# Kernel optimization log

Measured on AMD Instinct MI355X. Metric: run time of the kernel, lower is better.

Reference implementation:

```python
import jax, jax.numpy as jnp
import numpy as np
import math

ORDER = 4
FREQ = 160


def _layernorm(x, g, b, eps=1e-5):
    m = jnp.mean(x, axis=-1, keepdims=True)
    v = jnp.mean((x - m) ** 2, axis=-1, keepdims=True)
    return (x - m) / jnp.sqrt(v + eps) * g + b


def setup_inputs() -> dict:
    key = jax.random.key(0)
    ks = jax.random.split(key, 9)
    b, t, k, f = 8, 1000, ORDER, FREQ
    return {
        "far_complex": jax.random.normal(ks[0], (b, 2, f, t), jnp.float32),
        "mix_complex": jax.random.normal(ks[1], (b, 2, f, t), jnp.float32),
        "k_conv_w": jax.random.normal(ks[2], (2 * k, 2), jnp.float32) * 0.3,   # Conv2d(2 -> 2k, 1x1)
        "k_conv_b": jax.random.normal(ks[3], (2 * k,), jnp.float32) * 0.01,
        "ql_w": jax.random.normal(ks[4], (f, f), jnp.float32) / math.sqrt(f),  # query_linear
        "ql_b": jnp.zeros((f,), jnp.float32),
        "qn_g": jnp.ones((f,), jnp.float32),   # query_norm gamma
        "qn_b": jnp.zeros((f,), jnp.float32),  # query_norm beta
        "kl_w": jax.random.normal(ks[5], (k, k), jnp.float32) / math.sqrt(k),  # key_linear
        "kl_b": jnp.zeros((k,), jnp.float32),
        "kn_g": jnp.ones((k,), jnp.float32),
        "kn_b": jnp.zeros((k,), jnp.float32),
        "q_vec": jax.random.normal(ks[6], (f,), jnp.float32) * 0.5,  # query_vector
        "k_vec": jax.random.normal(ks[7], (k,), jnp.float32) * 0.5,  # key_vector
        "v_vec": jax.random.normal(ks[8], (k,), jnp.float32) * 0.5,  # value_vector
    }


def reference(far_complex, mix_complex, k_conv_w, k_conv_b, ql_w, ql_b,
              qn_g, qn_b, kl_w, kl_b, kn_g, kn_b, q_vec, k_vec, v_vec):
    b, c, f, t = far_complex.shape
    k = k_vec.shape[0]

    # im2col-style unfold over time with left padding (k-1)
    padded = jnp.pad(far_complex, ((0, 0), (0, 0), (0, 0), (k - 1, 0)))
    idx = jnp.arange(t)[:, None] + jnp.arange(k)[None, :]          # [t, k]
    unf = padded[..., idx]                                          # [b,2,f,t,k]
    unf_save = unf[:, 0] + 1j * unf[:, 1]                           # [b,f,t,k] complex64
    # in-place conjugation of imag channel (as in torch code)
    unf = jnp.stack([unf[:, 0], -unf[:, 1]], axis=1)                # [b,2,f,t,k]

    # per-channel outer products (torch does real matmul per channel)
    XTX = jnp.einsum('bcfti,bcftj->bcftij', unf, unf)               # [b,2,f,t,k,k]
    XTY = (unf * mix_complex[..., None])[..., None]                 # [b,2,f,t,k,1]

    query = jnp.transpose(unf, (0, 1, 3, 4, 2))                     # [b,2,t,k,f]
    kc = jnp.einsum('oc,bcft->boft', k_conv_w, mix_complex) + k_conv_b[None, :, None, None]
    key = jnp.transpose(kc.reshape(b, 2, k, f, t), (0, 1, 4, 3, 2))  # [b,2,t,f,k]

    value = jnp.swapaxes(jnp.concatenate([XTX, XTY], axis=-1), -1, -2)  # [b,2,f,t,k+1,k]

    query = _layernorm(query @ ql_w.T + ql_b, qn_g, qn_b) * jax.nn.sigmoid(q_vec)
    key = _layernorm(key @ kl_w.T + kl_b, kn_g, kn_b) * jax.nn.sigmoid(k_vec)
    value = value * jax.nn.sigmoid(v_vec)

    weight = jax.nn.softmax(query @ (key / math.sqrt(k)), axis=-1)  # [b,2,t,k,k]
    out = value @ weight[:, :, None]                                # [b,2,f,t,k+1,k]
    outT = jnp.swapaxes(out, -1, -2)                                # [b,2,f,t,k,k+1]
    XTX_new = outT[..., :k]                                         # [b,2,f,t,k,k]
    XTY_new = outT[..., k:]                                         # [b,2,f,t,k,1]
    XTX_c = XTX_new[:, 0] + 1j * XTX_new[:, 1]                      # [b,f,t,k,k]
    XTY_c = XTY_new[:, 0] + 1j * XTY_new[:, 1]                      # [b,f,t,k,1]

    eps = 1e-8
    eye_r = jnp.eye(k, dtype=jnp.float32) + eps
    eye = (eye_r + 1j * eye_r).astype(XTX_c.dtype)

    inv_XTX = jnp.linalg.inv(XTX_c + eye)                           # [b,f,t,k,k]
    wiener = (inv_XTX @ XTY_c)[..., 0]                              # [b,f,t,k]

    res = jnp.sum(unf_save * wiener, axis=-1)                       # [b,f,t]
    return jnp.stack([res.real, res.imag], axis=1)                  # [b,2,f,t]
```

## Files before the change

kernel.cpp:

```cpp
#include <hip/hip_runtime.h>
#include <math.h>

#define NBC   16
#define NF    160
#define NT    1000
#define TS    64
#define QSTR  81

typedef __attribute__((ext_vector_type(8))) short short8;
typedef __attribute__((ext_vector_type(4))) float f32x4;

static __device__ __forceinline__ short f2bf(float x) {
    unsigned u = __builtin_bit_cast(unsigned, x);
    unsigned r = (u + 0x7fffu + ((u >> 16) & 1u)) >> 16;
    return (short)r;
}
static __device__ __forceinline__ float bf2f(short s) {
    unsigned u = ((unsigned)(unsigned short)s) << 16;
    return __builtin_bit_cast(float, u);
}

__global__ __launch_bounds__(1024) void k13_fused(const float* __restrict__ far,
                                                  const float* __restrict__ mix,
                                                  const float* __restrict__ qlw,
                                                  const float* __restrict__ qlb,
                                                  const float* __restrict__ qng,
                                                  const float* __restrict__ qnb,
                                                  const float* __restrict__ qvec,
                                                  const float* __restrict__ kcw,
                                                  const float* __restrict__ kcb,
                                                  const float* __restrict__ klw,
                                                  const float* __restrict__ klb,
                                                  const float* __restrict__ kng,
                                                  const float* __restrict__ knb,
                                                  const float* __restrict__ kvec,
                                                  float* __restrict__ W) {
    __shared__ float pool[17600];
    __shared__ float lnM[80], lnI[80];
    float* Qlds = pool;
    float* redS = pool;
    float* redQ = pool + 3280;
    short* Bhi  = (short*)(pool + 12960);
    short* Blo  = (short*)(pool + 14240);
    float* sbuf = pool;

    const int bc = blockIdx.x;
    const int t0 = blockIdx.y * TS;
    const int tid = threadIdx.x;
    const int w = __builtin_amdgcn_readfirstlane(tid >> 6);
    const int l = tid & 63;
    const int b = bc >> 1, c = bc & 1;
    const float sgn = c ? -1.f : 1.f;
    const float* Xb = far + (size_t)bc * NF * NT;
    const int row = l & 15;
    const int kb = l >> 4;

    short8 Ahi[5], Alo[5];
    if (w < 10) {
        #pragma unroll
        for (int fc = 0; fc < 5; ++fc) {
            const float* ap = qlw + (size_t)(16 * w + row) * NF + fc * 32 + kb * 8;
            float4 x0 = *(const float4*)(ap + 0);
            float4 x1 = *(const float4*)(ap + 4);
            float xv[8] = {x0.x, x0.y, x0.z, x0.w, x1.x, x1.y, x1.z, x1.w};
            short8 h, lo;
            #pragma unroll
            for (int j = 0; j < 8; ++j) {
                short hj = f2bf(xv[j]);
                h[j] = hj;
                lo[j] = f2bf(xv[j] - bf2f(hj));
            }
            Ahi[fc] = h; Alo[fc] = lo;
        }
    }

    f32x4 acc0 = {0.f, 0.f, 0.f, 0.f}, acc1 = acc0, acc2 = acc0, acc3 = acc0, acc4 = acc0;
    float vcur0 = 0.f, vcur1 = 0.f, vcur2 = 0.f;

    #pragma unroll
    for (int i = 0; i < 3; ++i) {
        int e = tid + i * 1024;
        if (e < 2560) {
            int fi_l = e / 80, j = e - fi_l * 80;
            int tq = t0 - 3 + j;
            float v = (tq >= 0 && tq < NT) ? Xb[(size_t)fi_l * NT + tq] * sgn : 0.f;
            if (i == 0) vcur0 = v; else if (i == 1) vcur1 = v; else vcur2 = v;
        }
    }

    #pragma unroll
    for (int fc = 0; fc < 5; ++fc) {
        #pragma unroll
        for (int i = 0; i < 3; ++i) {
            int e = tid + i * 1024;
            if (e < 2560) {
                int fi_l = e / 80, j = e - fi_l * 80;
                int tt = j >> 4;
                int sl = ((fi_l >> 3) << 4) | (j & 15);
                int idx = (tt * 64 + sl) * 8 + (fi_l & 7);
                float v = (i == 0) ? vcur0 : (i == 1) ? vcur1 : vcur2;
                short hi = f2bf(v);
                Bhi[idx] = hi;
                Blo[idx] = f2bf(v - bf2f(hi));
            }
        }
        float vn0 = 0.f, vn1 = 0.f, vn2 = 0.f;
        if (fc < 4) {
            #pragma unroll
            for (int i = 0; i < 3; ++i) {
                int e = tid + i * 1024;
                if (e < 2560) {
                    int fi_l = e / 80, j = e - fi_l * 80;
                    int tq = t0 - 3 + j;
                    int fi = (fc + 1) * 32 + fi_l;
                    float v = (tq >= 0 && tq < NT) ? Xb[(size_t)fi * NT + tq] * sgn : 0.f;
                    if (i == 0) vn0 = v; else if (i == 1) vn1 = v; else vn2 = v;
                }
            }
        }
        __syncthreads();
        if (w < 10) {
            #pragma unroll
            for (int tt = 0; tt < 5; ++tt) {
                short8 bh = *(const short8*)&Bhi[(tt * 64 + l) * 8];
                short8 bl = *(const short8*)&Blo[(tt * 64 + l) * 8];
                f32x4 a = (tt == 0) ? acc0 : (tt == 1) ? acc1 : (tt == 2) ? acc2 : (tt == 3) ? acc3 : acc4;
                a = __builtin_amdgcn_mfma_f32_16x16x32_bf16(Ahi[fc], bh, a, 0, 0, 0);
                a = __builtin_amdgcn_mfma_f32_16x16x32_bf16(Ahi[fc], bl, a, 0, 0, 0);
                a = __builtin_amdgcn_mfma_f32_16x16x32_bf16(Alo[fc], bh, a, 0, 0, 0);
                if (tt == 0) acc0 = a; else if (tt == 1) acc1 = a; else if (tt == 2) acc2 = a;
                else if (tt == 3) acc3 = a; else acc4 = a;
            }
        }
        __syncthreads();
        vcur0 = vn0; vcur1 = vn1; vcur2 = vn2;
    }

    float qlbv[4], gam[4], bet[4];
    if (w < 10) {
        #pragma unroll
        for (int r = 0; r < 4; ++r) {
            int fo = 16 * w + kb * 4 + r;
            qlbv[r] = qlb[fo];
            float sq = 1.f / (1.f + expf(-qvec[fo]));
            gam[r] = qng[fo] * sq;
            bet[r] = qnb[fo] * sq;
        }
        #pragma unroll
        for (int tt = 0; tt < 5; ++tt) {
            f32x4 a = (tt == 0) ? acc0 : (tt == 1) ? acc1 : (tt == 2) ? acc2 : (tt == 3) ? acc3 : acc4;
            float v0 = a[0] + qlbv[0], v1 = a[1] + qlbv[1];
            float v2 = a[2] + qlbv[2], v3 = a[3] + qlbv[3];
            int j = tt * 16 + row;
            redS[j * 41 + w * 4 + kb] = v0 + v1 + v2 + v3;
            redQ[j * 41 + w * 4 + kb] = v0 * v0 + v1 * v1 + v2 * v2 + v3 * v3;
        }
    }
    __syncthreads();

    if (tid < 80) {
        float s = 0.f, q = 0.f;
        #pragma unroll 8
        for (int j = 0; j < 40; ++j) {
            s += redS[tid * 41 + j];
            q += redQ[tid * 41 + j];
        }
        float mean = s * (1.f / NF);
        float var = q * (1.f / NF) - mean * mean;
        lnM[tid] = mean;
        lnI[tid] = 1.f / sqrtf(var + 1e-5f);
    }
    __syncthreads();

    if (w < 10) {
        #pragma unroll
        for (int tt = 0; tt < 5; ++tt) {
            f32x4 a = (tt == 0) ? acc0 : (tt == 1) ? acc1 : (tt == 2) ? acc2 : (tt == 3) ? acc3 : acc4;
            int j = tt * 16 + row;
            float mean = lnM[j], inv = lnI[j];
            #pragma unroll
            for (int r = 0; r < 4; ++r) {
                int fo = 16 * w + kb * 4 + r;
                float v = a[r] + qlbv[r];
                Qlds[fo * QSTR + j] = (v - mean) * inv * gam[r] + bet[r];
            }
        }
    }
    __syncthreads();

    float alpha[4], beta4[4], gamm[4], G[4], H[4];
    {
        float M0[4], M1[4], B4[4];
        #pragma unroll
        for (int jo = 0; jo < 4; ++jo) {
            float m0 = 0.f, m1 = 0.f, bb = klb[jo];
            #pragma unroll
            for (int ji = 0; ji < 4; ++ji) {
                float kl = klw[jo * 4 + ji];
                m0 = fmaf(kl, kcw[(4 * c + ji) * 2 + 0], m0);
                m1 = fmaf(kl, kcw[(4 * c + ji) * 2 + 1], m1);
                bb = fmaf(kl, kcb[4 * c + ji], bb);
            }
            M0[jo] = m0; M1[jo] = m1; B4[jo] = bb;
        }
        float am = 0.25f * (M0[0] + M0[1] + M0[2] + M0[3]);
        float bm = 0.25f * (M1[0] + M1[1] + M1[2] + M1[3]);
        float cm = 0.25f * (B4[0] + B4[1] + B4[2] + B4[3]);
        #pragma unroll
        for (int jo = 0; jo < 4; ++jo) {
            alpha[jo] = M0[jo] - am;
            beta4[jo] = M1[jo] - bm;
            gamm[jo]  = B4[jo] - cm;
            float sk = 0.5f / (1.f + expf(-kvec[jo]));
            G[jo] = kng[jo] * sk;
            H[jo] = knb[jo] * sk;
        }
    }

    const int t = t0 + l;
    const bool valid = t < NT;

    float s[16];
    #pragma unroll
    for (int x = 0; x < 16; ++x) s[x] = 0.f;

    const float* mix0 = mix + (size_t)(b * 2) * NF * NT;
    const float* mix1 = mix0 + (size_t)NF * NT;
    const int f0 = w * 10;

    if (valid) {
        #pragma unroll
        for (int ff = 0; ff < 10; ++ff) {
            int f = f0 + ff;
            float m0 = mix0[(size_t)f * NT + t];
            float m1 = mix1[(size_t)f * NT + t];
            float d0 = fmaf(alpha[0], m0, fmaf(beta4[0], m1, gamm[0]));
            float d1 = fmaf(alpha[1], m0, fmaf(beta4[1], m1, gamm[1]));
            float d2 = fmaf(alpha[2], m0, fmaf(beta4[2], m1, gamm[2]));
            float d3 = fmaf(alpha[3], m0, fmaf(beta4[3], m1, gamm[3]));
            float var = 0.25f * (d0 * d0 + d1 * d1 + d2 * d2 + d3 * d3);
            float inv = 1.f / sqrtf(var + 1e-5f);
            float kn[4];
            kn[0] = fmaf(d0 * inv, G[0], H[0]);
            kn[1] = fmaf(d1 * inv, G[1], H[1]);
            kn[2] = fmaf(d2 * inv, G[2], H[2]);
            kn[3] = fmaf(d3 * inv, G[3], H[3]);

            float q0 = Qlds[f * QSTR + l + 0];
            float q1 = Qlds[f * QSTR + l + 1];
            float q2 = Qlds[f * QSTR + l + 2];
            float q3 = Qlds[f * QSTR + l + 3];
            #pragma unroll
            for (int j = 0; j < 4; ++j) {
                s[0 * 4 + j] = fmaf(q0, kn[j], s[0 * 4 + j]);
                s[1 * 4 + j] = fmaf(q1, kn[j], s[1 * 4 + j]);
                s[2 * 4 + j] = fmaf(q2, kn[j], s[2 * 4 + j]);
                s[3 * 4 + j] = fmaf(q3, kn[j], s[3 * 4 + j]);
            }
        }
    }
    __syncthreads();

    {
        float* dst = &sbuf[(w * 64 + l) * 17];
        #pragma unroll
        for (int q4 = 0; q4 < 4; ++q4) {
            float4 v = {s[q4 * 4 + 0], s[q4 * 4 + 1], s[q4 * 4 + 2], s[q4 * 4 + 3]};
            *(float4*)(dst + q4 * 4) = v;
        }
    }
    __syncthreads();

    if (tid < 256) {
        int q4 = tid >> 6;
        int ln = tid & 63;
        int tt = t0 + ln;
        if (tt < NT) {
            float4 a = *(const float4*)&sbuf[(0 * 64 + ln) * 17 + q4 * 4];
            #pragma unroll
            for (int ww = 1; ww < 16; ++ww) {
                float4 p = *(const float4*)&sbuf[(ww * 64 + ln) * 17 + q4 * 4];
                a.x += p.x; a.y += p.y; a.z += p.z; a.w += p.w;
            }
            float mx = fmaxf(fmaxf(a.x, a.y), fmaxf(a.z, a.w));
            float e0 = expf(a.x - mx), e1 = expf(a.y - mx);
            float e2 = expf(a.z - mx), e3 = expf(a.w - mx);
            float inv = 1.f / (e0 + e1 + e2 + e3);
            float4 v = {e0 * inv, e1 * inv, e2 * inv, e3 * inv};
            *(float4*)(W + ((size_t)bc * NT + tt) * 16 + q4 * 4) = v;
        }
    }
}

__device__ __forceinline__ void csolve4(float Ar[16], float Ai[16],
                                        float br[4], float bi[4],
                                        float wr[4], float wi[4]) {
    #pragma unroll
    for (int col = 0; col < 4; ++col) {
        #pragma unroll
        for (int r = col + 1; r < 4; ++r) {
            float cp = fabsf(Ar[col * 4 + col]) + fabsf(Ai[col * 4 + col]);
            float cr = fabsf(Ar[r * 4 + col]) + fabsf(Ai[r * 4 + col]);
            bool sw = cr > cp;
            #pragma unroll
            for (int m = col; m < 4; ++m) {
                float a0 = Ar[col * 4 + m], a1 = Ar[r * 4 + m];
                Ar[col * 4 + m] = sw ? a1 : a0;
                Ar[r * 4 + m]   = sw ? a0 : a1;
                float c0 = Ai[col * 4 + m], c1 = Ai[r * 4 + m];
                Ai[col * 4 + m] = sw ? c1 : c0;
                Ai[r * 4 + m]   = sw ? c0 : c1;
            }
            float b0 = br[col], b1 = br[r];
            br[col] = sw ? b1 : b0; br[r] = sw ? b0 : b1;
            float d0 = bi[col], d1 = bi[r];
            bi[col] = sw ? d1 : d0; bi[r] = sw ? d0 : d1;
        }
        float pr = Ar[col * 4 + col], pi = Ai[col * 4 + col];
        float den = 1.f / (pr * pr + pi * pi);
        #pragma unroll
        for (int r = col + 1; r < 4; ++r) {
            float nr = Ar[r * 4 + col], ni = Ai[r * 4 + col];
            float fr = (nr * pr + ni * pi) * den;
            float fi = (ni * pr - nr * pi) * den;
            #pragma unroll
            for (int m = col + 1; m < 4; ++m) {
                float tr = Ar[col * 4 + m], ti = Ai[col * 4 + m];
                Ar[r * 4 + m] -= fr * tr - fi * ti;
                Ai[r * 4 + m] -= fr * ti + fi * tr;
            }
            float tr = br[col], ti = bi[col];
            br[r] -= fr * tr - fi * ti;
            bi[r] -= fr * ti + fi * tr;
        }
    }
    #pragma unroll
    for (int col = 3; col >= 0; --col) {
        float sr = br[col], si = bi[col];
        #pragma unroll
        for (int m = col + 1; m < 4; ++m) {
            float tr = Ar[col * 4 + m], ti = Ai[col * 4 + m];
            sr -= tr * wr[m] - ti * wi[m];
            si -= tr * wi[m] + ti * wr[m];
        }
        float pr = Ar[col * 4 + col], pi = Ai[col * 4 + col];
        float den = 1.f / (pr * pr + pi * pi);
        wr[col] = (sr * pr + si * pi) * den;
        wi[col] = (si * pr - sr * pi) * den;
    }
}

__global__ __launch_bounds__(256) void k4_final(const float* __restrict__ far,
                                                const float* __restrict__ mix,
                                                const float* __restrict__ Wt,
                                                const float* __restrict__ vvec,
                                                float* __restrict__ out) {
    const int t = blockIdx.x * 256 + threadIdx.x;
    const int f = blockIdx.y;
    const int b = blockIdx.z;
    if (t >= NT) return;

    const float* fr  = far + (size_t)(b * 2 + 0) * NF * NT + (size_t)f * NT;
    const float* fim = far + (size_t)(b * 2 + 1) * NF * NT + (size_t)f * NT;
    float ur[4], ui[4];
    #pragma unroll
    for (int d = 0; d < 4; ++d) {
        int tp = t - 3 + d;
        bool ok = tp >= 0;
        ur[d] = ok ? fr[tp] : 0.f;
        ui[d] = ok ? fim[tp] : 0.f;
    }
    float m0 = mix[(size_t)(b * 2 + 0) * NF * NT + (size_t)f * NT + t];
    float m1 = mix[(size_t)(b * 2 + 1) * NF * NT + (size_t)f * NT + t];

    float sv[4];
    #pragma unroll
    for (int i = 0; i < 4; ++i) sv[i] = 1.f / (1.f + expf(-vvec[i]));

    const float* w0p = Wt + ((size_t)(b * 2 + 0) * NT + t) * 16;
    const float* w1p = Wt + ((size_t)(b * 2 + 1) * NT + t) * 16;

    float g0[4], g1[4];
    #pragma unroll
    for (int j = 0; j < 4; ++j) { g0[j] = 0.f; g1[j] = 0.f; }
    #pragma unroll
    for (int i = 0; i < 4; ++i) {
        float a0 = ur[i] * sv[i];
        float a1 = -ui[i] * sv[i];
        #pragma unroll
        for (int j = 0; j < 4; ++j) {
            g0[j] = fmaf(a0, w0p[i * 4 + j], g0[j]);
            g1[j] = fmaf(a1, w1p[i * 4 + j], g1[j]);
        }
    }

    float Ar[16], Ai[16], br[4], bi[4], wr[4], wi[4];
    #pragma unroll
    for (int j = 0; j < 4; ++j) {
        #pragma unroll
        for (int m = 0; m < 4; ++m) {
            float e = (j == m) ? (1.0f + 1e-8f) : 1e-8f;
            Ar[j * 4 + m] = fmaf(ur[m], g0[j], e);
            Ai[j * 4 + m] = fmaf(-ui[m], g1[j], e);
        }
        br[j] = m0 * g0[j];
        bi[j] = m1 * g1[j];
    }

    csolve4(Ar, Ai, br, bi, wr, wi);

    float resr = 0.f, resi = 0.f;
    #pragma unroll
    for (int d = 0; d < 4; ++d) {
        resr += ur[d] * wr[d] - ui[d] * wi[d];
        resi += ur[d] * wi[d] + ui[d] * wr[d];
    }
    out[(size_t)(b * 2 + 0) * NF * NT + (size_t)f * NT + t] = resr;
    out[(size_t)(b * 2 + 1) * NF * NT + (size_t)f * NT + t] = resi;
}

extern "C" void kernel_launch(void* const* d_in, const int* in_sizes, int n_in,
                              void* d_out, int out_size, void* d_ws, size_t ws_size,
                              hipStream_t stream) {
    const float* far  = (const float*)d_in[0];
    const float* mix  = (const float*)d_in[1];
    const float* kcw  = (const float*)d_in[2];
    const float* kcb  = (const float*)d_in[3];
    const float* qlw  = (const float*)d_in[4];
    const float* qlb  = (const float*)d_in[5];
    const float* qng  = (const float*)d_in[6];
    const float* qnb  = (const float*)d_in[7];
    const float* klw  = (const float*)d_in[8];
    const float* klb  = (const float*)d_in[9];
    const float* kng  = (const float*)d_in[10];
    const float* knb  = (const float*)d_in[11];
    const float* qvec = (const float*)d_in[12];
    const float* kvec = (const float*)d_in[13];
    const float* vvec = (const float*)d_in[14];

    float* W = (float*)d_ws;
    float* out = (float*)d_out;

    k13_fused<<<dim3(NBC, (NT + TS - 1) / TS), 1024, 0, stream>>>(
        far, mix, qlw, qlb, qng, qnb, qvec, kcw, kcb, klw, klb, kng, knb, kvec, W);
    k4_final<<<dim3(4, NF, 8), 256, 0, stream>>>(far, mix, W, vvec, out);
}
```

Before: 52.46 us.

## Factor query-key score into MFMA products over normalized mix channels

The per-thread FMA loop that built query-key scores from layer-normalised keys is replaced by an algebraic factorisation. Each score becomes a combination of three matrix products (Q times m0*inv, m1*inv and inv) plus a column sum of Q. Those products run on bf16 split-precision MFMA, and the block shrinks from 1024 to 640 threads so that every wave does MFMA work. The aim is to move the dominant score computation onto matrix cores and drop the 16-way LDS reduction, at the cost of more LDS staging, extra barriers and bf16 hi/lo split rounding.

```diff
diff --git a/kernel.cpp b/kernel.cpp
--- a/kernel.cpp
+++ b/kernel.cpp
@@ -5,7 +5,6 @@
 #define NF    160
 #define NT    1000
 #define TS    64
-#define QSTR  81
 
 typedef __attribute__((ext_vector_type(8))) short short8;
 typedef __attribute__((ext_vector_type(4))) float f32x4;
@@ -20,29 +19,32 @@
     return __builtin_bit_cast(float, u);
 }
 
-__global__ __launch_bounds__(1024) void k13_fused(const float* __restrict__ far,
-                                                  const float* __restrict__ mix,
-                                                  const float* __restrict__ qlw,
-                                                  const float* __restrict__ qlb,
-                                                  const float* __restrict__ qng,
-                                                  const float* __restrict__ qnb,
-                                                  const float* __restrict__ qvec,
-                                                  const float* __restrict__ kcw,
-                                                  const float* __restrict__ kcb,
-                                                  const float* __restrict__ klw,
-                                                  const float* __restrict__ klb,
-                                                  const float* __restrict__ kng,
-                                                  const float* __restrict__ knb,
-                                                  const float* __restrict__ kvec,
-                                                  float* __restrict__ W) {
-    __shared__ float pool[17600];
-    __shared__ float lnM[80], lnI[80];
+__global__ __launch_bounds__(640) void k13_fused(const float* __restrict__ far,
+                                                 const float* __restrict__ mix,
+                                                 const float* __restrict__ qlw,
+                                                 const float* __restrict__ qlb,
+                                                 const float* __restrict__ qng,
+                                                 const float* __restrict__ qnb,
+                                                 const float* __restrict__ qvec,
+                                                 const float* __restrict__ kcw,
+                                                 const float* __restrict__ kcb,
+                                                 const float* __restrict__ klw,
+                                                 const float* __restrict__ klb,
+                                                 const float* __restrict__ kng,
+                                                 const float* __restrict__ knb,
+                                                 const float* __restrict__ kvec,
+                                                 float* __restrict__ W) {
+    __shared__ float pool[19104];
+    __shared__ float lnM[80], lnI[80], cs[80];
+    __shared__ float psum[400];
     float* Qlds = pool;
     float* redS = pool;
     float* redQ = pool + 3280;
-    short* Bhi  = (short*)(pool + 12960);
-    short* Blo  = (short*)(pool + 14240);
-    float* sbuf = pool;
+    short* fBhi = (short*)(pool + 12960);
+    short* fBlo = fBhi + 2560;
+    short* MBhi = (short*)(pool + 12960);
+    short* MBlo = MBhi + 6144;
+    float* Dbuf = pool;
 
     const int bc = blockIdx.x;
     const int t0 = blockIdx.y * TS;
@@ -56,105 +58,71 @@
     const int kb = l >> 4;
 
     short8 Ahi[5], Alo[5];
-    if (w < 10) {
-        #pragma unroll
-        for (int fc = 0; fc < 5; ++fc) {
-            const float* ap = qlw + (size_t)(16 * w + row) * NF + fc * 32 + kb * 8;
-            float4 x0 = *(const float4*)(ap + 0);
-            float4 x1 = *(const float4*)(ap + 4);
-            float xv[8] = {x0.x, x0.y, x0.z, x0.w, x1.x, x1.y, x1.z, x1.w};
-            short8 h, lo;
-            #pragma unroll
-            for (int j = 0; j < 8; ++j) {
-                short hj = f2bf(xv[j]);
-                h[j] = hj;
-                lo[j] = f2bf(xv[j] - bf2f(hj));
-            }
-            Ahi[fc] = h; Alo[fc] = lo;
-        }
-    }
-
-    f32x4 acc0 = {0.f, 0.f, 0.f, 0.f}, acc1 = acc0, acc2 = acc0, acc3 = acc0, acc4 = acc0;
-    float vcur0 = 0.f, vcur1 = 0.f, vcur2 = 0.f;
-
-    #pragma unroll
-    for (int i = 0; i < 3; ++i) {
-        int e = tid + i * 1024;
-        if (e < 2560) {
+    #pragma unroll
+    for (int fc = 0; fc < 5; ++fc) {
+        const float* ap = qlw + (size_t)(16 * w + row) * NF + fc * 32 + kb * 8;
+        float4 x0 = *(const float4*)(ap + 0);
+        float4 x1 = *(const float4*)(ap + 4);
+        float xv[8] = {x0.x, x0.y, x0.z, x0.w, x1.x, x1.y, x1.z, x1.w};
+        short8 h, lo;
+        #pragma unroll
+        for (int j = 0; j < 8; ++j) {
+            short hj = f2bf(xv[j]);
+            h[j] = hj;
+            lo[j] = f2bf(xv[j] - bf2f(hj));
+        }
+        Ahi[fc] = h; Alo[fc] = lo;
+    }
+
+    f32x4 qa0 = {0.f, 0.f, 0.f, 0.f}, qa1 = qa0, qa2 = qa0, qa3 = qa0, qa4 = qa0;
+    #pragma unroll
+    for (int fc = 0; fc < 5; ++fc) {
+        #pragma unroll
+        for (int i = 0; i < 4; ++i) {
+            int e = tid + i * 640;
             int fi_l = e / 80, j = e - fi_l * 80;
             int tq = t0 - 3 + j;
-            float v = (tq >= 0 && tq < NT) ? Xb[(size_t)fi_l * NT + tq] * sgn : 0.f;
-            if (i == 0) vcur0 = v; else if (i == 1) vcur1 = v; else vcur2 = v;
-        }
-    }
-
-    #pragma unroll
-    for (int fc = 0; fc < 5; ++fc) {
-        #pragma unroll
-        for (int i = 0; i < 3; ++i) {
-            int e = tid + i * 1024;
-            if (e < 2560) {
-                int fi_l = e / 80, j = e - fi_l * 80;
-                int tt = j >> 4;
-                int sl = ((fi_l >> 3) << 4) | (j & 15);
-                int idx = (tt * 64 + sl) * 8 + (fi_l & 7);
-                float v = (i == 0) ? vcur0 : (i == 1) ? vcur1 : vcur2;
-                short hi = f2bf(v);
-                Bhi[idx] = hi;
-                Blo[idx] = f2bf(v - bf2f(hi));
-            }
-        }
-        float vn0 = 0.f, vn1 = 0.f, vn2 = 0.f;
-        if (fc < 4) {
-            #pragma unroll
-            for (int i = 0; i < 3; ++i) {
-                int e = tid + i * 1024;
-                if (e < 2560) {
-                    int fi_l = e / 80, j = e - fi_l * 80;
-                    int tq = t0 - 3 + j;
-                    int fi = (fc + 1) * 32 + fi_l;
-                    float v = (tq >= 0 && tq < NT) ? Xb[(size_t)fi * NT + tq] * sgn : 0.f;
-                    if (i == 0) vn0 = v; else if (i == 1) vn1 = v; else vn2 = v;
-                }
-            }
+            int fi = fc * 32 + fi_l;
+            float v = (tq >= 0 && tq < NT) ? Xb[(size_t)fi * NT + tq] * sgn : 0.f;
+            short hi = f2bf(v);
+            int tt = j >> 4;
+            int sl = ((fi_l >> 3) << 4) | (j & 15);
+            int idx = (tt * 64 + sl) * 8 + (fi_l & 7);
+            fBhi[idx] = hi;
+            fBlo[idx] = f2bf(v - bf2f(hi));
         }
         __syncthreads();
-        if (w < 10) {
-            #pragma unroll
-            for (int tt = 0; tt < 5; ++tt) {
-                short8 bh = *(const short8*)&Bhi[(tt * 64 + l) * 8];
-                short8 bl = *(const short8*)&Blo[(tt * 64 + l) * 8];
-                f32x4 a = (tt == 0) ? acc0 : (tt == 1) ? acc1 : (tt == 2) ? acc2 : (tt == 3) ? acc3 : acc4;
-                a = __builtin_amdgcn_mfma_f32_16x16x32_bf16(Ahi[fc], bh, a, 0, 0, 0);
-                a = __builtin_amdgcn_mfma_f32_16x16x32_bf16(Ahi[fc], bl, a, 0, 0, 0);
-                a = __builtin_amdgcn_mfma_f32_16x16x32_bf16(Alo[fc], bh, a, 0, 0, 0);
-                if (tt == 0) acc0 = a; else if (tt == 1) acc1 = a; else if (tt == 2) acc2 = a;
-                else if (tt == 3) acc3 = a; else acc4 = a;
-            }
+        #pragma unroll
+        for (int tt = 0; tt < 5; ++tt) {
+            short8 bh = *(const short8*)&fBhi[(tt * 64 + l) * 8];
+            short8 bl = *(const short8*)&fBlo[(tt * 64 + l) * 8];
+            f32x4 a = (tt == 0) ? qa0 : (tt == 1) ? qa1 : (tt == 2) ? qa2 : (tt == 3) ? qa3 : qa4;
+            a = __builtin_amdgcn_mfma_f32_16x16x32_bf16(Ahi[fc], bh, a, 0, 0, 0);
+            a = __builtin_amdgcn_mfma_f32_16x16x32_bf16(Ahi[fc], bl, a, 0, 0, 0);
+            a = __builtin_amdgcn_mfma_f32_16x16x32_bf16(Alo[fc], bh, a, 0, 0, 0);
+            if (tt == 0) qa0 = a; else if (tt == 1) qa1 = a; else if (tt == 2) qa2 = a;
+            else if (tt == 3) qa3 = a; else qa4 = a;
         }
         __syncthreads();
-        vcur0 = vn0; vcur1 = vn1; vcur2 = vn2;
     }
 
     float qlbv[4], gam[4], bet[4];
-    if (w < 10) {
-        #pragma unroll
-        for (int r = 0; r < 4; ++r) {
-            int fo = 16 * w + kb * 4 + r;
-            qlbv[r] = qlb[fo];
-            float sq = 1.f / (1.f + expf(-qvec[fo]));
-            gam[r] = qng[fo] * sq;
-            bet[r] = qnb[fo] * sq;
-        }
-        #pragma unroll
-        for (int tt = 0; tt < 5; ++tt) {
-            f32x4 a = (tt == 0) ? acc0 : (tt == 1) ? acc1 : (tt == 2) ? acc2 : (tt == 3) ? acc3 : acc4;
-            float v0 = a[0] + qlbv[0], v1 = a[1] + qlbv[1];
-            float v2 = a[2] + qlbv[2], v3 = a[3] + qlbv[3];
-            int j = tt * 16 + row;
-            redS[j * 41 + w * 4 + kb] = v0 + v1 + v2 + v3;
-            redQ[j * 41 + w * 4 + kb] = v0 * v0 + v1 * v1 + v2 * v2 + v3 * v3;
-        }
+    #pragma unroll
+    for (int r = 0; r < 4; ++r) {
+        int fo = 16 * w + kb * 4 + r;
+        qlbv[r] = qlb[fo];
+        float sq = 1.f / (1.f + expf(-qvec[fo]));
+        gam[r] = qng[fo] * sq;
+        bet[r] = qnb[fo] * sq;
+    }
+    #pragma unroll
+    for (int tt = 0; tt < 5; ++tt) {
+        f32x4 a = (tt == 0) ? qa0 : (tt == 1) ? qa1 : (tt == 2) ? qa2 : (tt == 3) ? qa3 : qa4;
+        float v0 = a[0] + qlbv[0], v1 = a[1] + qlbv[1];
+        float v2 = a[2] + qlbv[2], v3 = a[3] + qlbv[3];
+        int j = tt * 16 + row;
+        redS[j * 41 + w * 4 + kb] = v0 + v1 + v2 + v3;
+        redQ[j * 41 + w * 4 + kb] = v0 * v0 + v1 * v1 + v2 * v2 + v3 * v3;
     }
     __syncthreads();
 
@@ -172,20 +140,31 @@
     }
     __syncthreads();
 
-    if (w < 10) {
-        #pragma unroll
-        for (int tt = 0; tt < 5; ++tt) {
-            f32x4 a = (tt == 0) ? acc0 : (tt == 1) ? acc1 : (tt == 2) ? acc2 : (tt == 3) ? acc3 : acc4;
-            int j = tt * 16 + row;
-            float mean = lnM[j], inv = lnI[j];
-            #pragma unroll
-            for (int r = 0; r < 4; ++r) {
-                int fo = 16 * w + kb * 4 + r;
-                float v = a[r] + qlbv[r];
-                Qlds[fo * QSTR + j] = (v - mean) * inv * gam[r] + bet[r];
-            }
-        }
-    }
+    #pragma unroll
+    for (int tt = 0; tt < 5; ++tt) {
+        f32x4 a = (tt == 0) ? qa0 : (tt == 1) ? qa1 : (tt == 2) ? qa2 : (tt == 3) ? qa3 : qa4;
+        int j = tt * 16 + row;
+        float mean = lnM[j], inv = lnI[j];
+        #pragma unroll
+        for (int r = 0; r < 4; ++r) {
+            int fo = 16 * w + kb * 4 + r;
+            float v = a[r] + qlbv[r];
+            Qlds[fo * 81 + j] = (v - mean) * inv * gam[r] + bet[r];
+        }
+    }
+    __syncthreads();
+
+    if (tid < 400) {
+        int u = tid / 5, ch = tid - (tid / 5) * 5;
+        float s = 0.f;
+        #pragma unroll 8
+        for (int f = ch * 32; f < ch * 32 + 32; ++f) s += Qlds[f * 81 + u];
+        psum[tid] = s;
+    }
+    __syncthreads();
+    if (tid < 80)
+        cs[tid] = psum[tid * 5] + psum[tid * 5 + 1] + psum[tid * 5 + 2]
+                + psum[tid * 5 + 3] + psum[tid * 5 + 4];
     __syncthreads();
 
     float alpha[4], beta4[4], gamm[4], G[4], H[4];
@@ -217,77 +196,119 @@
         }
     }
 
-    const int t = t0 + l;
-    const bool valid = t < NT;
-
-    float s[16];
-    #pragma unroll
-    for (int x = 0; x < 16; ++x) s[x] = 0.f;
-
     const float* mix0 = mix + (size_t)(b * 2) * NF * NT;
     const float* mix1 = mix0 + (size_t)NF * NT;
-    const int f0 = w * 10;
-
-    if (valid) {
-        #pragma unroll
-        for (int ff = 0; ff < 10; ++ff) {
-            int f = f0 + ff;
-            float m0 = mix0[(size_t)f * NT + t];
-            float m1 = mix1[(size_t)f * NT + t];
-            float d0 = fmaf(alpha[0], m0, fmaf(beta4[0], m1, gamm[0]));
-            float d1 = fmaf(alpha[1], m0, fmaf(beta4[1], m1, gamm[1]));
-            float d2 = fmaf(alpha[2], m0, fmaf(beta4[2], m1, gamm[2]));
-            float d3 = fmaf(alpha[3], m0, fmaf(beta4[3], m1, gamm[3]));
-            float var = 0.25f * (d0 * d0 + d1 * d1 + d2 * d2 + d3 * d3);
-            float inv = 1.f / sqrtf(var + 1e-5f);
-            float kn[4];
-            kn[0] = fmaf(d0 * inv, G[0], H[0]);
-            kn[1] = fmaf(d1 * inv, G[1], H[1]);
-            kn[2] = fmaf(d2 * inv, G[2], H[2]);
-            kn[3] = fmaf(d3 * inv, G[3], H[3]);
-
-            float q0 = Qlds[f * QSTR + l + 0];
-            float q1 = Qlds[f * QSTR + l + 1];
-            float q2 = Qlds[f * QSTR + l + 2];
-            float q3 = Qlds[f * QSTR + l + 3];
+    const int ug = w % 5;
+    const int tgb = (w / 5) * 2;
+
+    f32x4 a00 = {0.f, 0.f, 0.f, 0.f}, a01 = a00;
+    f32x4 a10 = a00, a11 = a00;
+    f32x4 a20 = a00, a21 = a00;
+
+    #pragma unroll
+    for (int kc = 0; kc < 5; ++kc) {
+        #pragma unroll
+        for (int i = 0; i < 4; ++i) {
+            int e = tid + i * 640;
+            if (e < 2048) {
+                int f_l = e >> 6, tl = e & 63;
+                int t = t0 + tl;
+                int f = kc * 32 + f_l;
+                float m0 = 0.f, m1 = 0.f;
+                bool vt = t < NT;
+                if (vt) {
+                    m0 = mix0[(size_t)f * NT + t];
+                    m1 = mix1[(size_t)f * NT + t];
+                }
+                float d0 = fmaf(alpha[0], m0, fmaf(beta4[0], m1, gamm[0]));
+                float d1 = fmaf(alpha[1], m0, fmaf(beta4[1], m1, gamm[1]));
+                float d2 = fmaf(alpha[2], m0, fmaf(beta4[2], m1, gamm[2]));
+                float d3 = fmaf(alpha[3], m0, fmaf(beta4[3], m1, gamm[3]));
+                float var = 0.25f * (d0 * d0 + d1 * d1 + d2 * d2 + d3 * d3);
+                float inv = vt ? (1.f / sqrtf(var + 1e-5f)) : 0.f;
+                int tg = tl >> 4;
+                int sl = ((f_l >> 3) << 4) | (tl & 15);
+                int base = ((tg * 64 + sl) * 8) + (f_l & 7);
+                float v0m = m0 * inv, v1m = m1 * inv;
+                short h0 = f2bf(v0m), h1 = f2bf(v1m), h2 = f2bf(inv);
+                MBhi[base]        = h0;
+                MBhi[base + 2048] = h1;
+                MBhi[base + 4096] = h2;
+                MBlo[base]        = f2bf(v0m - bf2f(h0));
+                MBlo[base + 2048] = f2bf(v1m - bf2f(h1));
+                MBlo[base + 4096] = f2bf(inv - bf2f(h2));
+            }
+        }
+        __syncthreads();
+        short8 Ah, Al;
+        #pragma unroll
+        for (int jj = 0; jj < 8; ++jj) {
+            int f = kc * 32 + kb * 8 + jj;
+            float v = Qlds[f * 81 + ug * 16 + row];
+            short hj = f2bf(v);
+            Ah[jj] = hj;
+            Al[jj] = f2bf(v - bf2f(hj));
+        }
+        #pragma unroll
+        for (int mat = 0; mat < 3; ++mat) {
+            int s0 = (mat * 4 + tgb + 0) * 64 + l;
+            int s1 = (mat * 4 + tgb + 1) * 64 + l;
+            short8 bh0 = *(const short8*)&MBhi[s0 * 8];
+            short8 bl0 = *(const short8*)&MBlo[s0 * 8];
+            short8 bh1 = *(const short8*)&MBhi[s1 * 8];
+            short8 bl1 = *(const short8*)&MBlo[s1 * 8];
+            f32x4 a0 = (mat == 0) ? a00 : (mat == 1) ? a10 : a20;
+            f32x4 a1 = (mat == 0) ? a01 : (mat == 1) ? a11 : a21;
+            a0 = __builtin_amdgcn_mfma_f32_16x16x32_bf16(Ah, bh0, a0, 0, 0, 0);
+            a0 = __builtin_amdgcn_mfma_f32_16x16x32_bf16(Ah, bl0, a0, 0, 0, 0);
+            a0 = __builtin_amdgcn_mfma_f32_16x16x32_bf16(Al, bh0, a0, 0, 0, 0);
+            a1 = __builtin_amdgcn_mfma_f32_16x16x32_bf16(Ah, bh1, a1, 0, 0, 0);
+            a1 = __builtin_amdgcn_mfma_f32_16x16x32_bf16(Ah, bl1, a1, 0, 0, 0);
+            a1 = __builtin_amdgcn_mfma_f32_16x16x32_bf16(Al, bh1, a1, 0, 0, 0);
+            if (mat == 0) { a00 = a0; a01 = a1; }
+            else if (mat == 1) { a10 = a0; a11 = a1; }
+            else { a20 = a0; a21 = a1; }
+        }
+        __syncthreads();
+    }
+
+    #pragma unroll
+    for (int r = 0; r < 4; ++r) {
+        int u = ug * 16 + kb * 4 + r;
+        int tA = (tgb + 0) * 16 + row;
+        int tB = (tgb + 1) * 16 + row;
+        Dbuf[0 * 5280 + u * 66 + tA] = a00[r];
+        Dbuf[0 * 5280 + u * 66 + tB] = a01[r];
+        Dbuf[1 * 5280 + u * 66 + tA] = a10[r];
+        Dbuf[1 * 5280 + u * 66 + tB] = a11[r];
+        Dbuf[2 * 5280 + u * 66 + tA] = a20[r];
+        Dbuf[2 * 5280 + u * 66 + tB] = a21[r];
+    }
+    __syncthreads();
+
+    if (tid < 64) {
+        int ts = tid;
+        int t = t0 + ts;
+        if (t < NT) {
+            float* wp = W + ((size_t)bc * NT + t) * 16;
             #pragma unroll
-            for (int j = 0; j < 4; ++j) {
-                s[0 * 4 + j] = fmaf(q0, kn[j], s[0 * 4 + j]);
-                s[1 * 4 + j] = fmaf(q1, kn[j], s[1 * 4 + j]);
-                s[2 * 4 + j] = fmaf(q2, kn[j], s[2 * 4 + j]);
-                s[3 * 4 + j] = fmaf(q3, kn[j], s[3 * 4 + j]);
+            for (int q = 0; q < 4; ++q) {
+                int j = ts + q;
+                float csj = cs[j];
+                float A0 = Dbuf[0 * 5280 + j * 66 + ts];
+                float A1 = Dbuf[1 * 5280 + j * 66 + ts];
+                float A2 = Dbuf[2 * 5280 + j * 66 + ts];
+                float s0 = fmaf(G[0], fmaf(alpha[0], A0, fmaf(beta4[0], A1, gamm[0] * A2)), H[0] * csj);
+                float s1 = fmaf(G[1], fmaf(alpha[1], A0, fmaf(beta4[1], A1, gamm[1] * A2)), H[1] * csj);
+                float s2 = fmaf(G[2], fmaf(alpha[2], A0, fmaf(beta4[2], A1, gamm[2] * A2)), H[2] * csj);
+                float s3 = fmaf(G[3], fmaf(alpha[3], A0, fmaf(beta4[3], A1, gamm[3] * A2)), H[3] * csj);
+                float mx = fmaxf(fmaxf(s0, s1), fmaxf(s2, s3));
+                float e0 = expf(s0 - mx), e1 = expf(s1 - mx);
+                float e2 = expf(s2 - mx), e3 = expf(s3 - mx);
+                float inv = 1.f / (e0 + e1 + e2 + e3);
+                float4 v = {e0 * inv, e1 * inv, e2 * inv, e3 * inv};
+                *(float4*)(wp + q * 4) = v;
             }
-        }
-    }
-    __syncthreads();
-
-    {
-        float* dst = &sbuf[(w * 64 + l) * 17];
-        #pragma unroll
-        for (int q4 = 0; q4 < 4; ++q4) {
-            float4 v = {s[q4 * 4 + 0], s[q4 * 4 + 1], s[q4 * 4 + 2], s[q4 * 4 + 3]};
-            *(float4*)(dst + q4 * 4) = v;
-        }
-    }
-    __syncthreads();
-
-    if (tid < 256) {
-        int q4 = tid >> 6;
-        int ln = tid & 63;
-        int tt = t0 + ln;
-        if (tt < NT) {
-            float4 a = *(const float4*)&sbuf[(0 * 64 + ln) * 17 + q4 * 4];
-            #pragma unroll
-            for (int ww = 1; ww < 16; ++ww) {
-                float4 p = *(const float4*)&sbuf[(ww * 64 + ln) * 17 + q4 * 4];
-                a.x += p.x; a.y += p.y; a.z += p.z; a.w += p.w;
-            }
-            float mx = fmaxf(fmaxf(a.x, a.y), fmaxf(a.z, a.w));
-            float e0 = expf(a.x - mx), e1 = expf(a.y - mx);
-            float e2 = expf(a.z - mx), e3 = expf(a.w - mx);
-            float inv = 1.f / (e0 + e1 + e2 + e3);
-            float4 v = {e0 * inv, e1 * inv, e2 * inv, e3 * inv};
-            *(float4*)(W + ((size_t)bc * NT + tt) * 16 + q4 * 4) = v;
         }
     }
 }
@@ -441,7 +462,7 @@
     float* W = (float*)d_ws;
     float* out = (float*)d_out;
 
-    k13_fused<<<dim3(NBC, (NT + TS - 1) / TS), 1024, 0, stream>>>(
+    k13_fused<<<dim3(NBC, (NT + TS - 1) / TS), 640, 0, stream>>>(
         far, mix, qlw, qlb, qng, qnb, qvec, kcw, kcb, klw, klb, kng, knb, kvec, W);
     k4_final<<<dim3(4, NF, 8), 256, 0, stream>>>(far, mix, W, vvec, out);
 }
```

Measured after the change: 61.80 us. +17.8%, slower.
